# Performance work log

Hardware: AMD Instinct MI355X
Metric: run time of the kernel (lower is better)

Reference implementation:

```python
import jax, jax.numpy as jnp
import numpy as np

B, T, C = 1, 2048, 2048
H, G, HS = 32, 8, 64          # heads, query groups, head size
FF = 5632                     # LLaMAMLP intermediate size
EPS = 1e-5
LEVELS = 63.0                 # 2**6 - 1 (bit=6)


@jax.custom_vjp
def _uq(x, alpha):
    xd = x / alpha
    xq = jnp.round(jnp.clip(xd, 0.0, 1.0) * LEVELS) / LEVELS
    return xq * alpha


def _uq_fwd(x, alpha):
    xd = x / alpha
    xq = jnp.round(jnp.clip(xd, 0.0, 1.0) * LEVELS) / LEVELS
    return xq * alpha, (xd, xq)


def _uq_bwd(res, g):
    xd, xq = res
    i = (xd > 1.0).astype(g.dtype)
    grad_x = g * (1.0 - i)
    grad_alpha = jnp.sum(g * (i + (xq - xd) * (1.0 - i)))
    return grad_x, grad_alpha


_uq.defvjp(_uq_fwd, _uq_bwd)


def quant_relu(x, alpha):
    return _uq(jax.nn.relu(x), alpha)


def rmsnorm(x, w):
    return w * x * jax.lax.rsqrt(jnp.mean(x * x, axis=-1, keepdims=True) + EPS)


def setup_inputs() -> dict:
    key = jax.random.key(0)
    ks = jax.random.split(key, 8)
    s = 0.02
    shape_qkv = (H + 2 * G) * HS  # 3072
    return {
        "x": jax.random.normal(ks[0], (B, T, C), jnp.float32),
        "w_rms1": jnp.ones((C,), jnp.float32),
        "w_rms2": jnp.ones((C,), jnp.float32),
        "alpha1": jnp.asarray(8.0, jnp.float32),
        "alpha2": jnp.asarray(8.0, jnp.float32),
        "alpha_q": jnp.asarray(8.0, jnp.float32),
        "alpha_sm": jnp.asarray(8.0, jnp.float32),
        "attn_w": jax.random.normal(ks[1], (shape_qkv, C), jnp.float32) * s,
        "proj_w": jax.random.normal(ks[2], (C, C), jnp.float32) * s,
        "fc1_w": jax.random.normal(ks[3], (FF, C), jnp.float32) * s,
        "fc2_w": jax.random.normal(ks[4], (FF, C), jnp.float32) * s,
        "mlp_proj_w": jax.random.normal(ks[5], (C, FF), jnp.float32) * s,
        "max_seq_length": 2048,
    }


def _attention(n1, attn_w, proj_w, alpha_q, alpha_sm):
    q_per_kv = H // G
    qkv = quant_relu(jnp.einsum('btc,oc->bto', n1, attn_w), alpha_q)
    qkv = qkv.reshape(B, T, G, q_per_kv + 2, HS)
    q = qkv[..., :q_per_kv, :].reshape(B, T, H, HS)
    k = qkv[..., q_per_kv, :]      # [B,T,G,HS]
    v = qkv[..., q_per_kv + 1, :]  # [B,T,G,HS]
    k = jnp.repeat(k, q_per_kv, axis=2)  # [B,T,H,HS]
    v = jnp.repeat(v, q_per_kv, axis=2)
    scale = 1.0 / np.sqrt(HS).astype(np.float32)
    scores = jnp.einsum('bqhd,bkhd->bhqk', q, k) * scale
    causal = jnp.tril(jnp.ones((T, T), bool))
    scores = jnp.where(causal, scores, jnp.float32(-jnp.inf))
    w = jax.nn.softmax(scores, axis=-1)
    w = quant_relu(w, alpha_sm)  # quantized softmax weights (QuantReLU on probs)
    y = jnp.einsum('bhqk,bkhd->bqhd', w, v).reshape(B, T, C)
    return jnp.einsum('btc,oc->bto', y, proj_w)


def reference(x, w_rms1, w_rms2, alpha1, alpha2, attn_w, proj_w, alpha_q,
              alpha_sm, fc1_w, fc2_w, mlp_proj_w, max_seq_length):
    n1 = quant_relu(rmsnorm(x, w_rms1), alpha1)
    h = _attention(n1, attn_w, proj_w, alpha_q, alpha_sm)
    x = x + h
    n2 = quant_relu(rmsnorm(x, w_rms2), alpha2)
    gate = jax.nn.silu(jnp.einsum('btc,fc->btf', n2, fc1_w))
    up = jnp.einsum('btc,fc->btf', n2, fc2_w)
    mlp = jnp.einsum('btf,cf->btc', gate * up, mlp_proj_w)
    return x + mlp
```

## Files before the change

kernel.cpp:

```cpp
#include <hip/hip_runtime.h>
#include <hip/hip_bf16.h>
#include <math.h>


#define T_SEQ 2048
#define C_DIM 2048
#define QKV_DIM 3072
#define FF_DIM 5632
#define LOG2E 1.44269504088896340736f

typedef short bf16x8 __attribute__((ext_vector_type(8)));
typedef float f32x4 __attribute__((ext_vector_type(4)));
typedef unsigned int u32x4 __attribute__((ext_vector_type(4)));
typedef unsigned short u16;
typedef unsigned int u32;

__device__ __forceinline__ u16 f2bf(float f) {
  __hip_bfloat16 h = __float2bfloat16(f);
  return *reinterpret_cast<u16*>(&h);
}
__device__ __forceinline__ float bf2f(u16 u) {
  __hip_bfloat16 h;
  *reinterpret_cast<u16*>(&h) = u;
  return __bfloat162float(h);
}

__device__ __forceinline__ float qint(float v, float alpha) {
  float xd = fmaxf(v, 0.0f) / alpha;
  xd = fminf(xd, 1.0f);
  return rintf(xd * 63.0f);
}

__device__ __forceinline__ float exp2_hw(float x) {
  float r;
  asm("v_exp_f32 %0, %1" : "=v"(r) : "v"(x));
  return r;
}
__device__ __forceinline__ u32 cvtpk_bf16(float lo, float hi) {
  u32 r;
  asm("v_cvt_pk_bf16_f32 %0, %1, %2" : "=v"(r) : "v"(lo), "v"(hi));
  return r;
}

__device__ __forceinline__ void llds16(const void* g, void* l) {
  __builtin_amdgcn_global_load_lds(
      (const __attribute__((address_space(1))) unsigned int*)g,
      (__attribute__((address_space(3))) unsigned int*)l, 16, 0, 0);
}

__global__ __launch_bounds__(256) void rmsnorm_quant_int(const float* __restrict__ x,
                                                         const float* __restrict__ w,
                                                         const float* __restrict__ alpha_p,
                                                         u16* __restrict__ out) {
  const int row = blockIdx.x;
  const float* xr = x + (size_t)row * C_DIM;
  const int base = threadIdx.x * 8;
  float4 v0 = *reinterpret_cast<const float4*>(xr + base);
  float4 v1 = *reinterpret_cast<const float4*>(xr + base + 4);
  float xv[8] = {v0.x, v0.y, v0.z, v0.w, v1.x, v1.y, v1.z, v1.w};
  float ss = 0.0f;
#pragma unroll
  for (int k = 0; k < 8; ++k) ss = fmaf(xv[k], xv[k], ss);
#pragma unroll
  for (int m = 1; m < 64; m <<= 1) ss += __shfl_xor(ss, m);
  __shared__ float wsum[4];
  const int lane = threadIdx.x & 63, wv = threadIdx.x >> 6;
  if (lane == 0) wsum[wv] = ss;
  __syncthreads();
  const float tot = wsum[0] + wsum[1] + wsum[2] + wsum[3];
  const float rs = 1.0f / sqrtf(tot * (1.0f / 2048.0f) + 1e-5f);
  const float alpha = *alpha_p;
  u16 ov[8];
#pragma unroll
  for (int k = 0; k < 8; ++k) ov[k] = f2bf(qint((w[base + k] * xv[k]) * rs, alpha));
  u16* orow = out + (size_t)row * C_DIM + base;
#pragma unroll
  for (int k = 0; k < 2; ++k) {
    ushort4 u;
    u.x = ov[k * 4]; u.y = ov[k * 4 + 1]; u.z = ov[k * 4 + 2]; u.w = ov[k * 4 + 3];
    *reinterpret_cast<ushort4*>(orow + k * 4) = u;
  }
}

template <int MODE, int EPI>
__global__ __launch_bounds__(256) void gemm_mfma(
    const u16* __restrict__ A0, const u16* __restrict__ A1,
    const float* __restrict__ Bf,
    float* __restrict__ Cf, u16* __restrict__ Cq, const float* __restrict__ auxf,
    u16* __restrict__ p_hi, u16* __restrict__ p_lo,
    const float* __restrict__ sA_p, const float* __restrict__ aQ_p,
    int M, int N, int K) {
  constexpr int BUFB = (MODE == 2) ? 24576 : 32768;
  constexpr int BOFF = (MODE == 2) ? 8192 : 16384;
  __shared__ __align__(16) char lds[2 * BUFB];

  const int tid = threadIdx.x;
  const int nwg = gridDim.x * gridDim.y;
  const int wg = blockIdx.y * gridDim.x + blockIdx.x;
  const int swz = (wg & 7) * (nwg >> 3) + (wg >> 3);
  const int bx = swz % gridDim.x, by = swz / gridDim.x;
  const int row0 = by * 128, col0 = bx * 128;

  const int w = tid >> 6, lane = tid & 63;
  const int wr = w >> 1, wc = w & 1;
  const int fr = lane & 15, gq = lane >> 4;

  const int c0 = w * 128 + lane;
  const int r_a = c0 >> 2;
  const int s_a = (c0 & 3) * 8;
  const int rB = tid >> 3;
  const int sB0 = tid & 7;

  char* cu = lds;
  char* nx = lds + BUFB;

  auto stage = [&](char* base, int kt) {
    {
      const u16* g0 = A0 + (size_t)(row0 + r_a) * K + kt + s_a;
      const u16* g1 = A0 + (size_t)(row0 + r_a + 16) * K + kt + s_a;
      llds16(g0, base + (w * 128) * 16);
      llds16(g1, base + (w * 128 + 64) * 16);
    }
    if constexpr (MODE == 3) {
      const u16* g0 = A1 + (size_t)(row0 + r_a) * K + kt + s_a;
      const u16* g1 = A1 + (size_t)(row0 + r_a + 16) * K + kt + s_a;
      llds16(g0, base + 8192 + (w * 128) * 16);
      llds16(g1, base + 8192 + (w * 128 + 64) * 16);
    }
#pragma unroll
    for (int it = 0; it < 4; ++it) {
      const int rowB = it * 32 + rB;
      const int slot = sB0 ^ (rowB & 7);
      const float* gp = Bf + (size_t)(col0 + rowB) * K + kt + slot * 4;
      llds16(gp, base + BOFF + it * 4096 + w * 1024);
    }
  };

  f32x4 acc[4][4];
  const f32x4 zero = {0.f, 0.f, 0.f, 0.f};
#pragma unroll
  for (int m = 0; m < 4; ++m)
#pragma unroll
    for (int n = 0; n < 4; ++n) acc[m][n] = zero;

  stage(cu, 0);
  __syncthreads();

  for (int kt = 0;; kt += 32) {
    const bool more = (kt + 32 < K);
    if (more) stage(nx, kt + 32);

    const char* bufA = cu;
    const char* bufB = cu + BOFF;
    bf16x8 a0f[4], bhf[4], blf[4];
#pragma unroll
    for (int m = 0; m < 4; ++m)
      a0f[m] = *reinterpret_cast<const bf16x8*>(
          bufA + (wr * 64 + m * 16 + fr) * 64 + gq * 16);
#pragma unroll
    for (int n = 0; n < 4; ++n) {
      const int rowB = wc * 64 + n * 16 + fr;
      const int bb = rowB * 128 + gq * 32;
      const int sw = (rowB & 7) << 4;
      f32x4 e0 = *reinterpret_cast<const f32x4*>(bufB + (bb ^ sw));
      f32x4 e1 = *reinterpret_cast<const f32x4*>(bufB + ((bb + 16) ^ sw));
      float e[8] = {e0[0], e0[1], e0[2], e0[3], e1[0], e1[1], e1[2], e1[3]};
      u32 hp[4], lp[4];
#pragma unroll
      for (int p = 0; p < 4; ++p) {
        const u32 u0 = __builtin_bit_cast(u32, e[2 * p]);
        const u32 u1 = __builtin_bit_cast(u32, e[2 * p + 1]);
        hp[p] = (u1 & 0xffff0000u) | (u0 >> 16);
        const float l0 = e[2 * p]     - __builtin_bit_cast(float, u0 & 0xffff0000u);
        const float l1 = e[2 * p + 1] - __builtin_bit_cast(float, u1 & 0xffff0000u);
        lp[p] = cvtpk_bf16(l0, l1);
      }
      u32x4 hv = {hp[0], hp[1], hp[2], hp[3]};
      u32x4 lv = {lp[0], lp[1], lp[2], lp[3]};
      bhf[n] = __builtin_bit_cast(bf16x8, hv);
      blf[n] = __builtin_bit_cast(bf16x8, lv);
    }
    if constexpr (MODE == 2) {
#pragma unroll
      for (int m = 0; m < 4; ++m)
#pragma unroll
        for (int n = 0; n < 4; ++n) {
          acc[m][n] = __builtin_amdgcn_mfma_f32_16x16x32_bf16(a0f[m], bhf[n], acc[m][n], 0, 0, 0);
          acc[m][n] = __builtin_amdgcn_mfma_f32_16x16x32_bf16(a0f[m], blf[n], acc[m][n], 0, 0, 0);
        }
    } else {
      bf16x8 a1f[4];
#pragma unroll
      for (int m = 0; m < 4; ++m)
        a1f[m] = *reinterpret_cast<const bf16x8*>(
            cu + 8192 + (wr * 64 + m * 16 + fr) * 64 + gq * 16);
#pragma unroll
      for (int m = 0; m < 4; ++m)
#pragma unroll
        for (int n = 0; n < 4; ++n) {
          acc[m][n] = __builtin_amdgcn_mfma_f32_16x16x32_bf16(a0f[m], bhf[n], acc[m][n], 0, 0, 0);
          acc[m][n] = __builtin_amdgcn_mfma_f32_16x16x32_bf16(a1f[m], bhf[n], acc[m][n], 0, 0, 0);
          acc[m][n] = __builtin_amdgcn_mfma_f32_16x16x32_bf16(a0f[m], blf[n], acc[m][n], 0, 0, 0);
        }
    }
    if (!more) break;
    __syncthreads();
    char* t = cu; cu = nx; nx = t;
  }

  float sA = 1.0f, aQ = 1.0f;
  if constexpr (EPI == 1) { sA = (*sA_p) * (1.0f / 63.0f); aQ = *aQ_p; }
  if constexpr (EPI == 2 || EPI == 3) { sA = (*sA_p) * (1.0f / 63.0f); }
#pragma unroll
  for (int m = 0; m < 4; ++m)
#pragma unroll
    for (int n = 0; n < 4; ++n) {
      const int gcol = col0 + wc * 64 + n * 16 + fr;
#pragma unroll
      for (int j = 0; j < 4; ++j) {
        const int grow = row0 + wr * 64 + m * 16 + (lane >> 4) * 4 + j;
        const size_t idx = (size_t)grow * N + gcol;
        const float v = acc[m][n][j];
        if constexpr (EPI == 0) {
          Cf[idx] = auxf[idx] + v;
        } else if constexpr (EPI == 1) {
          float t = v * sA;
          float xd = fminf(fmaxf(t, 0.0f) / aQ, 1.0f);
          Cq[idx] = f2bf(rintf(xd * 63.0f));
        } else if constexpr (EPI == 2) {
          float t = v * sA;
          u16 h = f2bf(t);
          p_hi[idx] = h;
          p_lo[idx] = f2bf(t - bf2f(h));
        } else if constexpr (EPI == 3) {
          float gg = bf2f(p_hi[idx]) + bf2f(p_lo[idx]);
          float u = v * sA;
          float gu = (gg / (1.0f + expf(-gg))) * u;
          u16 h = f2bf(gu);
          p_hi[idx] = h;
          p_lo[idx] = f2bf(gu - bf2f(h));
        }
      }
    }
}

__global__ __launch_bounds__(256) void v_transpose(const u16* __restrict__ qkv,
                                                   u16* __restrict__ vt) {
  const int tb = blockIdx.x, g = blockIdx.y;
  const int vcol = (g * 6 + 5) * 64;
  __shared__ u16 t[64][72];
  const int tid = threadIdx.x;
#pragma unroll
  for (int i = 0; i < 2; ++i) {
    const int ch = i * 256 + tid;
    const int row = ch >> 3, c8 = (ch & 7) * 8;
    bf16x8 v = *reinterpret_cast<const bf16x8*>(
        qkv + (size_t)(tb * 64 + row) * QKV_DIM + vcol + c8);
#pragma unroll
    for (int j = 0; j < 8; ++j) t[c8 + j][row] = (u16)v[j];
  }
  __syncthreads();
#pragma unroll
  for (int i = 0; i < 2; ++i) {
    const int ch = i * 256 + tid;
    const int hs = ch >> 3, t8 = (ch & 7) * 8;
    ushort4 a, b;
    a.x = t[hs][t8];     a.y = t[hs][t8 + 1]; a.z = t[hs][t8 + 2]; a.w = t[hs][t8 + 3];
    b.x = t[hs][t8 + 4]; b.y = t[hs][t8 + 5]; b.z = t[hs][t8 + 6]; b.w = t[hs][t8 + 7];
    u16* dst = vt + (size_t)(g * 64 + hs) * T_SEQ + tb * 64 + t8;
    *reinterpret_cast<ushort4*>(dst) = a;
    *reinterpret_cast<ushort4*>(dst + 4) = b;
  }
}

__global__ __launch_bounds__(256) void attn_fused(const u16* __restrict__ qkv,
                                                  const u16* __restrict__ vt,
                                                  u16* __restrict__ y_hi,
                                                  u16* __restrict__ y_lo,
                                                  const float* __restrict__ aq_p,
                                                  const float* __restrict__ asm_p) {
  const int c = blockIdx.x;
  const int chi = c >> 8, mid = (c >> 4) & 15, clo = c & 15;
  const int h = mid + (chi << 4);
  const int qb = chi ? (15 - clo) : clo;
  const int g = h >> 2, s = h & 3;
  const int q_col = (g * 6 + s) * 64;
  const int k_col = (g * 6 + 4) * 64;

  __shared__ __align__(16) char lds_raw[49152];
  u16* Ks  = (u16*)(lds_raw + 16384);
  u16* Vts = (u16*)(lds_raw + 24576);

  const int tid = threadIdx.x;
  const int w = tid >> 6, lane = tid & 63;
  const int fr = lane & 15, gg = lane >> 4;
  char* myW = lds_raw + 32768 + w * 4096;

  const float sq = (*aq_p) * (1.0f / 63.0f);
  const float scale2 = sq * sq * 0.125f * LOG2E;
  const float alpha_sm = *asm_p;
  const float inv_a63 = 63.0f / alpha_sm;
  const float scale_y = (alpha_sm * (1.0f / 63.0f)) * sq;
  const int nkt = 2 * qb + 2;

#pragma unroll
  for (int i = 0; i < 4; ++i) {
    const int cb = (w * 4 + i) * 64;
    const int ch = cb + lane;
    const int row = ch >> 3;
    const int sb = ((ch & 7) * 16) ^ ((row & 7) << 4);
    llds16(qkv + (size_t)(qb * 128 + row) * QKV_DIM + q_col + (sb >> 1),
           lds_raw + cb * 16);
  }
  __syncthreads();
  bf16x8 qf[2][2];
#pragma unroll
  for (int nq = 0; nq < 2; ++nq)
#pragma unroll
    for (int ks = 0; ks < 2; ++ks) {
      const int qr = w * 32 + nq * 16 + fr;
      qf[nq][ks] = *reinterpret_cast<const bf16x8*>(
          lds_raw + ((qr * 128 + ks * 64 + gg * 16) ^ ((qr & 7) << 4)));
    }

  float m_run[2] = {-INFINITY, -INFINITY};
  float l_run[2] = {0.0f, 0.0f};

  for (int kt = 0; kt < nkt; ++kt) {
    __syncthreads();
#pragma unroll
    for (int i = 0; i < 2; ++i) {
      const int cb = (w * 2 + i) * 64;
      const int ch = cb + lane;
      const int row = ch >> 3;
      const int sb = ((ch & 7) * 16) ^ ((row & 7) << 4);
      llds16(qkv + (size_t)(kt * 64 + row) * QKV_DIM + k_col + (sb >> 1),
             (char*)Ks + cb * 16);
    }
    __syncthreads();
    f32x4 sac[4][2];
    const f32x4 zero = {0.f, 0.f, 0.f, 0.f};
#pragma unroll
    for (int mk = 0; mk < 4; ++mk)
#pragma unroll
      for (int nq = 0; nq < 2; ++nq) sac[mk][nq] = zero;
#pragma unroll
    for (int ks = 0; ks < 2; ++ks)
#pragma unroll
      for (int mk = 0; mk < 4; ++mk) {
        const int kr = mk * 16 + fr;
        bf16x8 kf = *reinterpret_cast<const bf16x8*>(
            (char*)Ks + ((kr * 128 + ks * 64 + gg * 16) ^ ((kr & 7) << 4)));
#pragma unroll
        for (int nq = 0; nq < 2; ++nq)
          sac[mk][nq] = __builtin_amdgcn_mfma_f32_16x16x32_bf16(kf, qf[nq][ks], sac[mk][nq], 0, 0, 0);
      }
    const bool edge = (kt >= 2 * qb);
#pragma unroll
    for (int nq = 0; nq < 2; ++nq) {
      const int qglob = qb * 128 + w * 32 + nq * 16 + fr;
      float tv[16];
#pragma unroll
      for (int mk = 0; mk < 4; ++mk)
#pragma unroll
        for (int jj = 0; jj < 4; ++jj) {
          float t = sac[mk][nq][jj] * scale2;
          if (edge && (kt * 64 + mk * 16 + gg * 4 + jj > qglob)) t = -INFINITY;
          tv[mk * 4 + jj] = t;
        }
      float vm = tv[0];
#pragma unroll
      for (int i = 1; i < 16; ++i) vm = fmaxf(vm, tv[i]);
      vm = fmaxf(vm, __shfl_xor(vm, 16));
      vm = fmaxf(vm, __shfl_xor(vm, 32));
      const float mn = fmaxf(m_run[nq], vm);
      float p = 0.0f;
#pragma unroll
      for (int i = 0; i < 16; ++i) p += exp2_hw(tv[i] - mn);
      p += __shfl_xor(p, 16);
      p += __shfl_xor(p, 32);
      l_run[nq] = l_run[nq] * exp2_hw(m_run[nq] - mn) + p;
      m_run[nq] = mn;
    }
  }

  const float linv[2] = {1.0f / l_run[0], 1.0f / l_run[1]};
  f32x4 oac[4][2];
  {
    const f32x4 zero = {0.f, 0.f, 0.f, 0.f};
#pragma unroll
    for (int mh = 0; mh < 4; ++mh)
#pragma unroll
      for (int nq = 0; nq < 2; ++nq) oac[mh][nq] = zero;
  }

  for (int kt = 0; kt < nkt; ++kt) {
    __syncthreads();
#pragma unroll
    for (int i = 0; i < 2; ++i) {
      const int cb = (w * 2 + i) * 64;
      const int ch = cb + lane;
      const int row = ch >> 3;
      const int sb = ((ch & 7) * 16) ^ ((row & 7) << 4);
      llds16(qkv + (size_t)(kt * 64 + row) * QKV_DIM + k_col + (sb >> 1),
             (char*)Ks + cb * 16);
      llds16(vt + (size_t)(g * 64 + row) * T_SEQ + kt * 64 + (sb >> 1),
             (char*)Vts + cb * 16);
    }
    __syncthreads();
    f32x4 sac[4][2];
    const f32x4 zero = {0.f, 0.f, 0.f, 0.f};
#pragma unroll
    for (int mk = 0; mk < 4; ++mk)
#pragma unroll
      for (int nq = 0; nq < 2; ++nq) sac[mk][nq] = zero;
#pragma unroll
    for (int ks = 0; ks < 2; ++ks)
#pragma unroll
      for (int mk = 0; mk < 4; ++mk) {
        const int kr = mk * 16 + fr;
        bf16x8 kf = *reinterpret_cast<const bf16x8*>(
            (char*)Ks + ((kr * 128 + ks * 64 + gg * 16) ^ ((kr & 7) << 4)));
#pragma unroll
        for (int nq = 0; nq < 2; ++nq)
          sac[mk][nq] = __builtin_amdgcn_mfma_f32_16x16x32_bf16(kf, qf[nq][ks], sac[mk][nq], 0, 0, 0);
      }
    const bool edge = (kt >= 2 * qb);
#pragma unroll
    for (int nq = 0; nq < 2; ++nq) {
      const int qglob = qb * 128 + w * 32 + nq * 16 + fr;
      const int qloc = nq * 16 + fr;
      const float mr = m_run[nq];
      const float cw = linv[nq] * inv_a63;
#pragma unroll
      for (int mk = 0; mk < 4; ++mk) {
        float lv[4];
#pragma unroll
        for (int jj = 0; jj < 4; ++jj) {
          float t = sac[mk][nq][jj] * scale2;
          if (edge && (kt * 64 + mk * 16 + gg * 4 + jj > qglob)) t = -INFINITY;
          lv[jj] = rintf(fminf(exp2_hw(t - mr) * cw, 63.0f));
        }
        const u32 pk0 = cvtpk_bf16(lv[0], lv[1]);
        const u32 pk1 = cvtpk_bf16(lv[2], lv[3]);
        const int b0 = (qloc * 128 + (mk * 16 + gg * 4) * 2) ^ ((qloc & 7) << 4);
        *reinterpret_cast<u32*>(myW + b0) = pk0;
        *reinterpret_cast<u32*>(myW + b0 + 4) = pk1;
      }
    }
#pragma unroll
    for (int ks = 0; ks < 2; ++ks) {
      bf16x8 wf[2];
#pragma unroll
      for (int nq = 0; nq < 2; ++nq) {
        const int qloc = nq * 16 + fr;
        wf[nq] = *reinterpret_cast<const bf16x8*>(
            myW + ((qloc * 128 + ks * 64 + gg * 16) ^ ((qloc & 7) << 4)));
      }
#pragma unroll
      for (int mh = 0; mh < 4; ++mh) {
        const int hr = mh * 16 + fr;
        bf16x8 vf = *reinterpret_cast<const bf16x8*>(
            (char*)Vts + ((hr * 128 + ks * 64 + gg * 16) ^ ((hr & 7) << 4)));
#pragma unroll
        for (int nq = 0; nq < 2; ++nq)
          oac[mh][nq] = __builtin_amdgcn_mfma_f32_16x16x32_bf16(vf, wf[nq], oac[mh][nq], 0, 0, 0);
      }
    }
  }

  __syncthreads();
  float* osc = (float*)(lds_raw + w * 8192);
#pragma unroll
  for (int mh = 0; mh < 4; ++mh)
#pragma unroll
    for (int nq = 0; nq < 2; ++nq) {
      const int qloc = nq * 16 + fr;
#pragma unroll
      for (int jj = 0; jj < 4; ++jj) {
        const int hs = mh * 16 + gg * 4 + jj;
        *reinterpret_cast<float*>(
            (char*)osc + ((qloc * 256 + hs * 4) ^ ((qloc & 7) << 4))) =
            oac[mh][nq][jj] * scale_y;
      }
    }
  __syncthreads();
  const int qp = lane >> 1, hf = lane & 1;
  const int qrow = qb * 128 + w * 32 + qp;
  u16* dh = y_hi + (size_t)qrow * C_DIM + h * 64 + hf * 32;
  u16* dl = y_lo + (size_t)qrow * C_DIM + h * 64 + hf * 32;
#pragma unroll
  for (int u = 0; u < 8; ++u) {
    f32x4 v = *reinterpret_cast<const f32x4*>(
        (char*)osc + ((qp * 256 + hf * 128 + u * 16) ^ ((qp & 7) << 4)));
    ushort4 hh, ll;
    u16 t0 = f2bf(v[0]); hh.x = t0; ll.x = f2bf(v[0] - bf2f(t0));
    u16 t1 = f2bf(v[1]); hh.y = t1; ll.y = f2bf(v[1] - bf2f(t1));
    u16 t2 = f2bf(v[2]); hh.z = t2; ll.z = f2bf(v[2] - bf2f(t2));
    u16 t3 = f2bf(v[3]); hh.w = t3; ll.w = f2bf(v[3] - bf2f(t3));
    *reinterpret_cast<ushort4*>(dh + u * 4) = hh;
    *reinterpret_cast<ushort4*>(dl + u * 4) = ll;
  }
}

extern "C" void kernel_launch(void* const* d_in, const int* in_sizes, int n_in,
                              void* d_out, int out_size, void* d_ws, size_t ws_size,
                              hipStream_t stream) {
  (void)in_sizes; (void)n_in; (void)out_size; (void)ws_size;
  const float* x      = (const float*)d_in[0];
  const float* w1     = (const float*)d_in[1];
  const float* w2     = (const float*)d_in[2];
  const float* a1     = (const float*)d_in[3];
  const float* a2     = (const float*)d_in[4];
  const float* aq     = (const float*)d_in[5];
  const float* a_sm   = (const float*)d_in[6];
  const float* attn_w = (const float*)d_in[7];
  const float* proj_w = (const float*)d_in[8];
  const float* fc1_w  = (const float*)d_in[9];
  const float* fc2_w  = (const float*)d_in[10];
  const float* mlp_w  = (const float*)d_in[11];
  float* out = (float*)d_out;

  char* ws = (char*)d_ws;
  u16* nb    = (u16*)ws;
  char* R    = ws + 8388608;
  u16* qkv_i = (u16*)R;
  u16* y_hi  = (u16*)(R + 12582912);
  u16* y_lo  = (u16*)(R + 20971520);
  u16* vt    = (u16*)(R + 29360128);
  u16* ghi   = (u16*)R;
  u16* glo   = (u16*)(R + 23068672);

  rmsnorm_quant_int<<<T_SEQ, 256, 0, stream>>>(x, w1, a1, nb);
  gemm_mfma<2, 1><<<dim3(QKV_DIM / 128, T_SEQ / 128), 256, 0, stream>>>(
      nb, nullptr, attn_w, nullptr, qkv_i, nullptr, nullptr, nullptr,
      a1, aq, T_SEQ, QKV_DIM, C_DIM);
  v_transpose<<<dim3(32, 8), 256, 0, stream>>>(qkv_i, vt);
  attn_fused<<<512, 256, 0, stream>>>(qkv_i, vt, y_hi, y_lo, aq, a_sm);
  gemm_mfma<3, 0><<<dim3(C_DIM / 128, T_SEQ / 128), 256, 0, stream>>>(
      y_hi, y_lo, proj_w, out, nullptr, x, nullptr, nullptr,
      nullptr, nullptr, T_SEQ, C_DIM, C_DIM);
  rmsnorm_quant_int<<<T_SEQ, 256, 0, stream>>>(out, w2, a2, nb);
  gemm_mfma<2, 2><<<dim3(FF_DIM / 128, T_SEQ / 128), 256, 0, stream>>>(
      nb, nullptr, fc1_w, nullptr, nullptr, nullptr, ghi, glo,
      a2, nullptr, T_SEQ, FF_DIM, C_DIM);
  gemm_mfma<2, 3><<<dim3(FF_DIM / 128, T_SEQ / 128), 256, 0, stream>>>(
      nb, nullptr, fc2_w, nullptr, nullptr, nullptr, ghi, glo,
      a2, nullptr, T_SEQ, FF_DIM, C_DIM);
  gemm_mfma<3, 0><<<dim3(C_DIM / 128, T_SEQ / 128), 256, 0, stream>>>(
      ghi, glo, mlp_w, out, nullptr, out, nullptr, nullptr,
      nullptr, nullptr, T_SEQ, C_DIM, FF_DIM);
}
```

Measured before the change: 995.8 us.

## Parameterize GEMM M-tile, swizzle A tile in LDS, add MFMA priority hints

Templates the GEMM on the M tile size and uses BM=64 for the QKV, attention-projection and MLP-down GEMMs. This doubles their grid so the 256 CUs are better covered. It also adds an XOR swizzle to the A-operand layout in LDS to reduce bank conflicts on fragment reads. The attention kernel raises wave priority around its MFMA blocks with s_setprio. Smaller tiles reload B more often relative to compute, which may cost bandwidth.

Result: no change. 1.008 ms (+1.2%).

```diff
diff --git a/kernel.cpp b/kernel.cpp
--- a/kernel.cpp
+++ b/kernel.cpp
@@ -82,7 +82,7 @@
   }
 }
 
-template <int MODE, int EPI>
+template <int MODE, int EPI, int BM>
 __global__ __launch_bounds__(256) void gemm_mfma(
     const u16* __restrict__ A0, const u16* __restrict__ A1,
     const float* __restrict__ Bf,
@@ -90,8 +90,11 @@
     u16* __restrict__ p_hi, u16* __restrict__ p_lo,
     const float* __restrict__ sA_p, const float* __restrict__ aQ_p,
     int M, int N, int K) {
-  constexpr int BUFB = (MODE == 2) ? 24576 : 32768;
-  constexpr int BOFF = (MODE == 2) ? 8192 : 16384;
+  constexpr int APL  = BM * 64;
+  constexpr int BOFF = (MODE == 3 ? 2 : 1) * APL;
+  constexpr int BUFB = BOFF + 16384;
+  constexpr int WRT  = BM / 2;
+  constexpr int MF   = WRT / 16;
   __shared__ __align__(16) char lds[2 * BUFB];
 
   const int tid = threadIdx.x;
@@ -99,15 +102,15 @@
   const int wg = blockIdx.y * gridDim.x + blockIdx.x;
   const int swz = (wg & 7) * (nwg >> 3) + (wg >> 3);
   const int bx = swz % gridDim.x, by = swz / gridDim.x;
-  const int row0 = by * 128, col0 = bx * 128;
+  const int row0 = by * BM, col0 = bx * 128;
 
   const int w = tid >> 6, lane = tid & 63;
   const int wr = w >> 1, wc = w & 1;
   const int fr = lane & 15, gq = lane >> 4;
 
-  const int c0 = w * 128 + lane;
-  const int r_a = c0 >> 2;
-  const int s_a = (c0 & 3) * 8;
+  const int cA = w * BM + lane;
+  const int rA = cA >> 2;
+  const int sAsw = ((cA & 3) ^ (rA & 3)) * 8;
   const int rB = tid >> 3;
   const int sB0 = tid & 7;
 
@@ -116,16 +119,20 @@
 
   auto stage = [&](char* base, int kt) {
     {
-      const u16* g0 = A0 + (size_t)(row0 + r_a) * K + kt + s_a;
-      const u16* g1 = A0 + (size_t)(row0 + r_a + 16) * K + kt + s_a;
-      llds16(g0, base + (w * 128) * 16);
-      llds16(g1, base + (w * 128 + 64) * 16);
+      const u16* g0 = A0 + (size_t)(row0 + rA) * K + kt + sAsw;
+      llds16(g0, base + (w * BM) * 16);
+      if constexpr (BM == 128) {
+        const u16* g1 = A0 + (size_t)(row0 + rA + 16) * K + kt + sAsw;
+        llds16(g1, base + (w * BM + 64) * 16);
+      }
     }
     if constexpr (MODE == 3) {
-      const u16* g0 = A1 + (size_t)(row0 + r_a) * K + kt + s_a;
-      const u16* g1 = A1 + (size_t)(row0 + r_a + 16) * K + kt + s_a;
-      llds16(g0, base + 8192 + (w * 128) * 16);
-      llds16(g1, base + 8192 + (w * 128 + 64) * 16);
+      const u16* g0 = A1 + (size_t)(row0 + rA) * K + kt + sAsw;
+      llds16(g0, base + APL + (w * BM) * 16);
+      if constexpr (BM == 128) {
+        const u16* g1 = A1 + (size_t)(row0 + rA + 16) * K + kt + sAsw;
+        llds16(g1, base + APL + (w * BM + 64) * 16);
+      }
     }
 #pragma unroll
     for (int it = 0; it < 4; ++it) {
@@ -136,10 +143,10 @@
     }
   };
 
-  f32x4 acc[4][4];
+  f32x4 acc[MF][4];
   const f32x4 zero = {0.f, 0.f, 0.f, 0.f};
 #pragma unroll
-  for (int m = 0; m < 4; ++m)
+  for (int m = 0; m < MF; ++m)
 #pragma unroll
     for (int n = 0; n < 4; ++n) acc[m][n] = zero;
 
@@ -152,11 +159,13 @@
 
     const char* bufA = cu;
     const char* bufB = cu + BOFF;
-    bf16x8 a0f[4], bhf[4], blf[4];
-#pragma unroll
-    for (int m = 0; m < 4; ++m)
+    bf16x8 a0f[MF], bhf[4], blf[4];
+#pragma unroll
+    for (int m = 0; m < MF; ++m) {
+      const int ar = wr * WRT + m * 16 + fr;
       a0f[m] = *reinterpret_cast<const bf16x8*>(
-          bufA + (wr * 64 + m * 16 + fr) * 64 + gq * 16);
+          bufA + ((ar * 64 + gq * 16) ^ ((ar & 3) << 4)));
+    }
 #pragma unroll
     for (int n = 0; n < 4; ++n) {
       const int rowB = wc * 64 + n * 16 + fr;
@@ -182,20 +191,22 @@
     }
     if constexpr (MODE == 2) {
 #pragma unroll
-      for (int m = 0; m < 4; ++m)
+      for (int m = 0; m < MF; ++m)
 #pragma unroll
         for (int n = 0; n < 4; ++n) {
           acc[m][n] = __builtin_amdgcn_mfma_f32_16x16x32_bf16(a0f[m], bhf[n], acc[m][n], 0, 0, 0);
           acc[m][n] = __builtin_amdgcn_mfma_f32_16x16x32_bf16(a0f[m], blf[n], acc[m][n], 0, 0, 0);
         }
     } else {
-      bf16x8 a1f[4];
-#pragma unroll
-      for (int m = 0; m < 4; ++m)
+      bf16x8 a1f[MF];
+#pragma unroll
+      for (int m = 0; m < MF; ++m) {
+        const int ar = wr * WRT + m * 16 + fr;
         a1f[m] = *reinterpret_cast<const bf16x8*>(
-            cu + 8192 + (wr * 64 + m * 16 + fr) * 64 + gq * 16);
-#pragma unroll
-      for (int m = 0; m < 4; ++m)
+            cu + APL + ((ar * 64 + gq * 16) ^ ((ar & 3) << 4)));
+      }
+#pragma unroll
+      for (int m = 0; m < MF; ++m)
 #pragma unroll
         for (int n = 0; n < 4; ++n) {
           acc[m][n] = __builtin_amdgcn_mfma_f32_16x16x32_bf16(a0f[m], bhf[n], acc[m][n], 0, 0, 0);
@@ -212,13 +223,13 @@
   if constexpr (EPI == 1) { sA = (*sA_p) * (1.0f / 63.0f); aQ = *aQ_p; }
   if constexpr (EPI == 2 || EPI == 3) { sA = (*sA_p) * (1.0f / 63.0f); }
 #pragma unroll
-  for (int m = 0; m < 4; ++m)
+  for (int m = 0; m < MF; ++m)
 #pragma unroll
     for (int n = 0; n < 4; ++n) {
       const int gcol = col0 + wc * 64 + n * 16 + fr;
 #pragma unroll
       for (int j = 0; j < 4; ++j) {
-        const int grow = row0 + wr * 64 + m * 16 + (lane >> 4) * 4 + j;
+        const int grow = row0 + wr * WRT + m * 16 + (lane >> 4) * 4 + j;
         const size_t idx = (size_t)grow * N + gcol;
         const float v = acc[m][n][j];
         if constexpr (EPI == 0) {
@@ -344,6 +355,7 @@
     for (int mk = 0; mk < 4; ++mk)
 #pragma unroll
       for (int nq = 0; nq < 2; ++nq) sac[mk][nq] = zero;
+    __builtin_amdgcn_s_setprio(1);
 #pragma unroll
     for (int ks = 0; ks < 2; ++ks)
 #pragma unroll
@@ -355,6 +367,7 @@
         for (int nq = 0; nq < 2; ++nq)
           sac[mk][nq] = __builtin_amdgcn_mfma_f32_16x16x32_bf16(kf, qf[nq][ks], sac[mk][nq], 0, 0, 0);
       }
+    __builtin_amdgcn_s_setprio(0);
     const bool edge = (kt >= 2 * qb);
 #pragma unroll
     for (int nq = 0; nq < 2; ++nq) {
@@ -414,6 +427,7 @@
     for (int mk = 0; mk < 4; ++mk)
 #pragma unroll
       for (int nq = 0; nq < 2; ++nq) sac[mk][nq] = zero;
+    __builtin_amdgcn_s_setprio(1);
 #pragma unroll
     for (int ks = 0; ks < 2; ++ks)
 #pragma unroll
@@ -425,6 +439,7 @@
         for (int nq = 0; nq < 2; ++nq)
           sac[mk][nq] = __builtin_amdgcn_mfma_f32_16x16x32_bf16(kf, qf[nq][ks], sac[mk][nq], 0, 0, 0);
       }
+    __builtin_amdgcn_s_setprio(0);
     const bool edge = (kt >= 2 * qb);
 #pragma unroll
     for (int nq = 0; nq < 2; ++nq) {
@@ -448,6 +463,7 @@
         *reinterpret_cast<u32*>(myW + b0 + 4) = pk1;
       }
     }
+    __builtin_amdgcn_s_setprio(1);
 #pragma unroll
     for (int ks = 0; ks < 2; ++ks) {
       bf16x8 wf[2];
@@ -467,6 +483,7 @@
           oac[mh][nq] = __builtin_amdgcn_mfma_f32_16x16x32_bf16(vf, wf[nq], oac[mh][nq], 0, 0, 0);
       }
     }
+    __builtin_amdgcn_s_setprio(0);
   }
 
   __syncthreads();
@@ -532,22 +549,22 @@
   u16* glo   = (u16*)(R + 23068672);
 
   rmsnorm_quant_int<<<T_SEQ, 256, 0, stream>>>(x, w1, a1, nb);
-  gemm_mfma<2, 1><<<dim3(QKV_DIM / 128, T_SEQ / 128), 256, 0, stream>>>(
+  gemm_mfma<2, 1, 64><<<dim3(QKV_DIM / 128, T_SEQ / 64), 256, 0, stream>>>(
       nb, nullptr, attn_w, nullptr, qkv_i, nullptr, nullptr, nullptr,
       a1, aq, T_SEQ, QKV_DIM, C_DIM);
   v_transpose<<<dim3(32, 8), 256, 0, stream>>>(qkv_i, vt);
   attn_fused<<<512, 256, 0, stream>>>(qkv_i, vt, y_hi, y_lo, aq, a_sm);
-  gemm_mfma<3, 0><<<dim3(C_DIM / 128, T_SEQ / 128), 256, 0, stream>>>(
+  gemm_mfma<3, 0, 64><<<dim3(C_DIM / 128, T_SEQ / 64), 256, 0, stream>>>(
       y_hi, y_lo, proj_w, out, nullptr, x, nullptr, nullptr,
       nullptr, nullptr, T_SEQ, C_DIM, C_DIM);
   rmsnorm_quant_int<<<T_SEQ, 256, 0, stream>>>(out, w2, a2, nb);
-  gemm_mfma<2, 2><<<dim3(FF_DIM / 128, T_SEQ / 128), 256, 0, stream>>>(
+  gemm_mfma<2, 2, 128><<<dim3(FF_DIM / 128, T_SEQ / 128), 256, 0, stream>>>(
       nb, nullptr, fc1_w, nullptr, nullptr, nullptr, ghi, glo,
       a2, nullptr, T_SEQ, FF_DIM, C_DIM);
-  gemm_mfma<2, 3><<<dim3(FF_DIM / 128, T_SEQ / 128), 256, 0, stream>>>(
+  gemm_mfma<2, 3, 128><<<dim3(FF_DIM / 128, T_SEQ / 128), 256, 0, stream>>>(
       nb, nullptr, fc2_w, nullptr, nullptr, nullptr, ghi, glo,
       a2, nullptr, T_SEQ, FF_DIM, C_DIM);
-  gemm_mfma<3, 0><<<dim3(C_DIM / 128, T_SEQ / 128), 256, 0, stream>>>(
+  gemm_mfma<3, 0, 64><<<dim3(C_DIM / 128, T_SEQ / 64), 256, 0, stream>>>(
       ghi, glo, mlp_w, out, nullptr, out, nullptr, nullptr,
       nullptr, nullptr, T_SEQ, C_DIM, FF_DIM);
 }
```
